# Kernel optimization log

Hardware: AMD Instinct MI355X
Metric: run time of the kernel (lower is better)

Reference implementation:

```python
import jax, jax.numpy as jnp
import numpy as np

B = 4096      # sessions
L = 32        # tokens per session (constant so sum(seq_len) == T)
T = B * L     # total tokens
H = 128       # hidden_size
HI = 8 * H    # input embedding dim (hidden_size * 8)


def setup_inputs() -> dict:
    key = jax.random.key(0)
    ks = jax.random.split(key, 8)
    s = lambda k, shape: jax.random.normal(k, shape, dtype=jnp.float32) * 0.02
    return {
        "inter_item_emb": s(ks[0], (T, HI)),
        "intra_item_emb": s(ks[1], (T, HI)),
        "seq_len": jnp.full((B,), L, dtype=jnp.int32),
        "Wf1_w": s(ks[2], (H, HI)), "Wf1_b": jnp.zeros((H,), jnp.float32),
        "Wf2_w": s(ks[3], (H, HI)), "Wf2_b": jnp.zeros((H,), jnp.float32),
        "W1_w": s(ks[4], (H, H)),   "W1_b": jnp.zeros((H,), jnp.float32),
        "W2_w": s(ks[5], (H, H)),   "W2_b": jnp.zeros((H,), jnp.float32),
        "q_w": s(ks[6], (1, H)),    "q_b": jnp.zeros((1,), jnp.float32),
        "W3_w": s(ks[7], (H, 2 * H)), "W3_b": jnp.zeros((H,), jnp.float32),
    }


def reference(inter_item_emb, intra_item_emb, seq_len,
              Wf1_w, Wf1_b, Wf2_w, Wf2_b,
              W1_w, W1_b, W2_w, W2_b,
              q_w, q_b, W3_w, W3_b):
    lin = lambda x, w, b: x @ w.T + b  # torch nn.Linear convention

    # item fusing: gated combination of the two projected embeddings
    f1 = lin(inter_item_emb, Wf1_w, Wf1_b)          # [T, H]
    f2 = lin(intra_item_emb, Wf2_w, Wf2_b)          # [T, H]
    gate = jax.nn.sigmoid(f1 + f2)
    h = f1 * gate + f2 * (1.0 - gate)               # [T, H]

    Ttok = h.shape[0]
    nseg = seq_len.shape[0]
    ends = jnp.cumsum(seq_len)                      # [B] exclusive ends
    # segment id of each token (sessions are contiguous row blocks)
    seg = jnp.searchsorted(ends, jnp.arange(Ttok), side="right")  # [T]
    last_idx = ends - 1                             # [B] last token of each session
    v_n = h[last_idx]                               # [B, H]

    # attention: alpha = q(sigmoid(W1(v_n_repeat) + W2(h)))
    w1v = lin(v_n, W1_w, W1_b)                      # [B, H], gather instead of repeat
    alpha = lin(jax.nn.sigmoid(w1v[seg] + lin(h, W2_w, W2_b)), q_w, q_b)  # [T, 1]

    # attention-weighted segment sum pooling
    s_g = jax.ops.segment_sum(alpha * h, seg, num_segments=nseg)  # [B, H]

    h_s = lin(jnp.concatenate([v_n, s_g], axis=1), W3_w, W3_b)    # [B, H]
    return h_s
```

## Files before the change

kernel.cpp:

```cpp
#include <hip/hip_runtime.h>
#include <hip/hip_bf16.h>

#define THREADS 512
#define HP 136

typedef float f32x4 __attribute__((ext_vector_type(4)));
typedef short s16x8 __attribute__((ext_vector_type(8)));

static __device__ __forceinline__ short f2b(float x) {
    return __builtin_bit_cast(short, __float2bfloat16(x));
}
static __device__ __forceinline__ float b2f(short u) {
    unsigned int v = ((unsigned int)(unsigned short)u) << 16;
    return __builtin_bit_cast(float, v);
}
static __device__ __forceinline__ void split8(const f32x4 a, const f32x4 b, s16x8& hi, s16x8& lo) {
    #pragma unroll
    for (int j = 0; j < 4; ++j) {
        short h0 = f2b(a[j]); hi[j]   = h0; lo[j]   = f2b(a[j] - b2f(h0));
        short h1 = f2b(b[j]); hi[j+4] = h1; lo[j+4] = f2b(b[j] - b2f(h1));
    }
}
static __device__ __forceinline__ s16x8 cvt8(const f32x4 a, const f32x4 b) {
    s16x8 r;
    r[0]=f2b(a[0]); r[1]=f2b(a[1]); r[2]=f2b(a[2]); r[3]=f2b(a[3]);
    r[4]=f2b(b[0]); r[5]=f2b(b[1]); r[6]=f2b(b[2]); r[7]=f2b(b[3]);
    return r;
}
static __device__ __forceinline__ float sigm(float x) { return 1.0f / (1.0f + __expf(-x)); }

#define MFMA16(A,B,C) __builtin_amdgcn_mfma_f32_16x16x32_bf16((A),(B),(C),0,0,0)

#define RAWBAR() do {                                               \
    asm volatile("s_waitcnt lgkmcnt(0)" ::: "memory");              \
    __builtin_amdgcn_s_barrier();                                   \
    asm volatile("" ::: "memory"); } while (0)

__global__ __launch_bounds__(256) void itemfusing_prep(
    const float* __restrict__ Wf1, const float* __restrict__ Wf2,
    const float* __restrict__ W2, short* __restrict__ wsp)
{
    const int t = blockIdx.x * 256 + threadIdx.x;
    if (t < 32768) {
        const int s  = t & 7;
        const int n  = (t >> 3) & 127;
        const int kc = (t >> 10) & 15;
        const int fz = (t >> 14) & 1;
        const int k  = kc * 64 + (s >> 2) * 32 + (s & 3) * 8;
        const float* src = (fz ? Wf2 : Wf1) + (size_t)n * 1024 + k;
        const int sp = s ^ (n & 7);
        *(s16x8*)(wsp + (size_t)(fz * 16 + kc) * 8192 + n * 64 + sp * 8)
            = cvt8(*(const f32x4*)src, *(const f32x4*)(src + 4));
    } else if (t < 32768 + 2048) {
        const int i = (t - 32768) * 8;
        const float* src = W2 + i;
        *(s16x8*)(wsp + 262144 + i) = cvt8(*(const f32x4*)src, *(const f32x4*)(src + 4));
    }
}

__global__ __launch_bounds__(THREADS, 2) void itemfusing_main(
    const float* __restrict__ inter, const float* __restrict__ intra,
    const float* __restrict__ bf1, const float* __restrict__ bf2,
    const float* __restrict__ W1,  const float* __restrict__ b1,
    const float* __restrict__ b2,
    const float* __restrict__ qw,  const float* __restrict__ qb,
    const float* __restrict__ W3,  const float* __restrict__ b3,
    const short* __restrict__ gimg, const short* __restrict__ w2b,
    float* __restrict__ out)
{
    __shared__ union {
        short wbuf[2][2][128][64];
        struct {
            short hbuf[4][32][HP];
            float vn [8][128];
            float w1v[8][128];
            float sgl[8][128];
        } t;
    } u;

    const int tid = threadIdx.x;
    const int w   = tid >> 6;
    const int l   = tid & 63;
    const int l15 = l & 15;
    const int kg  = l >> 4;
    const int sess = blockIdx.x * 8 + w;
    const int row0 = sess * 32;
    const int m7  = l15 & 7;
    const int s0p = (kg ^ m7) * 8;
    const int s1p = ((4 + kg) ^ m7) * 8;

    const float* A1 = inter + (size_t)(row0 + l15) * 1024 + kg * 8;
    const float* A2 = intra + (size_t)(row0 + l15) * 1024 + kg * 8;
    short* wb = &u.wbuf[0][0][0][0];

    f32x4 acc1[2][8], acc2[2][8];
    #pragma unroll
    for (int mt = 0; mt < 2; ++mt)
        #pragma unroll
        for (int nt = 0; nt < 8; ++nt) {
            acc1[mt][nt] = f32x4{0.f,0.f,0.f,0.f};
            acc2[mt][nt] = f32x4{0.f,0.f,0.f,0.f};
        }

    s16x8 wr0, wr1, wr2, wr3;
#define WLOADR(KC) do {                                                         \
    const short* p0_ = gimg + (size_t)(KC) * 8192 + tid * 8;                    \
    const short* p1_ = gimg + (size_t)(16 + (KC)) * 8192 + tid * 8;             \
    wr0 = *(const s16x8*)p0_;          wr1 = *(const s16x8*)(p0_ + 4096);       \
    wr2 = *(const s16x8*)p1_;          wr3 = *(const s16x8*)(p1_ + 4096); } while (0)
#define WSTORE(BUF) do {                                                        \
    short* d_ = wb + (BUF) * 16384 + tid * 8;                                   \
    *(s16x8*)d_ = wr0;           *(s16x8*)(d_ + 4096) = wr1;                    \
    *(s16x8*)(d_ + 8192) = wr2;  *(s16x8*)(d_ + 12288) = wr3; } while (0)

    f32x4 AE0, AE1, AE2, AE3, AE4, AE5, AE6, AE7;
    f32x4 AO0, AO1, AO2, AO3, AO4, AO5, AO6, AO7;
#define ALOAD(S, AP, KC) do {                                                   \
    const float* p_ = (AP) + (KC) * 64;                                         \
    S##0 = *(const f32x4*)p_;        S##1 = *(const f32x4*)(p_ + 4);            \
    S##2 = *(const f32x4*)(p_ + 32); S##3 = *(const f32x4*)(p_ + 36);           \
    const float* q_ = p_ + (size_t)16 * 1024;                                   \
    S##4 = *(const f32x4*)q_;        S##5 = *(const f32x4*)(q_ + 4);            \
    S##6 = *(const f32x4*)(q_ + 32); S##7 = *(const f32x4*)(q_ + 36); } while (0)

#define KSTEP(PB, ACC, AH0, AH1, AL0, AL1, SP) do {                             \
    _Pragma("unroll")                                                           \
    for (int nt_ = 0; nt_ < 8; ++nt_) {                                         \
        s16x8 bh_ = *(const s16x8*)((PB) + nt_ * 1024 + (SP));                  \
        ACC[0][nt_] = MFMA16(AH0, bh_, ACC[0][nt_]);                            \
        ACC[1][nt_] = MFMA16(AH1, bh_, ACC[1][nt_]);                            \
        ACC[0][nt_] = MFMA16(AL0, bh_, ACC[0][nt_]);                            \
        ACC[1][nt_] = MFMA16(AL1, bh_, ACC[1][nt_]);                            \
    } } while (0)

#define COMPUTE(BUF, FZ, ACC, S) do {                                           \
    const short* pb_ = wb + (BUF) * 16384 + (FZ) * 8192 + l15 * 64;             \
    s16x8 ah0, al0, ah1, al1;                                                   \
    split8(S##0, S##1, ah0, al0);                                               \
    split8(S##4, S##5, ah1, al1);                                               \
    KSTEP(pb_, ACC, ah0, ah1, al0, al1, s0p);                                   \
    split8(S##2, S##3, ah0, al0);                                               \
    split8(S##6, S##7, ah1, al1);                                               \
    KSTEP(pb_, ACC, ah0, ah1, al0, al1, s1p);                                   \
    } while (0)

    WLOADR(0); WSTORE(0);
    WLOADR(1);
    ALOAD(AE, A1, 0);
    ALOAD(AO, A2, 0);
    RAWBAR();

    #pragma unroll 1
    for (int kc = 0; kc < 16; ++kc) {
        const bool more = (kc < 15);
        if (more) WSTORE((kc + 1) & 1);
        if (kc < 14) WLOADR(kc + 2);
        COMPUTE(kc & 1, 0, acc1, AE);
        if (more) ALOAD(AE, A1, kc + 1);
        COMPUTE(kc & 1, 1, acc2, AO);
        if (more) ALOAD(AO, A2, kc + 1);
        RAWBAR();
    }
#undef WLOADR
#undef WSTORE
#undef ALOAD
#undef KSTEP
#undef COMPUTE

    #pragma unroll
    for (int nt = 0; nt < 8; ++nt) {
        const int n = nt * 16 + l15;
        const float bb1 = bf1[n], bb2 = bf2[n];
        #pragma unroll
        for (int mt = 0; mt < 2; ++mt)
            #pragma unroll
            for (int rj = 0; rj < 4; ++rj) {
                float x1 = acc1[mt][nt][rj] + bb1;
                float x2 = acc2[mt][nt][rj] + bb2;
                float g  = sigm(x1 + x2);
                acc1[mt][nt][rj] = x2 + g * (x1 - x2);
            }
    }

    if (kg == 3) {
        #pragma unroll
        for (int nt = 0; nt < 8; ++nt) u.t.vn[w][nt * 16 + l15] = acc1[1][nt][3];
    }
    asm volatile("s_waitcnt lgkmcnt(0)" ::: "memory");

    {
        const int n0 = l, n1 = l + 64;
        const float* w1r0 = W1 + (size_t)n0 * 128;
        const float* w1r1 = W1 + (size_t)n1 * 128;
        float s0 = 0.f, s1 = 0.f;
        #pragma unroll
        for (int kk = 0; kk < 128; kk += 4) {
            f32x4 vv = *(const f32x4*)&u.t.vn[w][kk];
            f32x4 u0 = *(const f32x4*)(w1r0 + kk);
            f32x4 u1 = *(const f32x4*)(w1r1 + kk);
            #pragma unroll
            for (int j = 0; j < 4; ++j) { s0 += u0[j] * vv[j]; s1 += u1[j] * vv[j]; }
        }
        u.t.w1v[w][n0] = s0 + b1[n0];
        u.t.w1v[w][n1] = s1 + b1[n1];
    }
    asm volatile("s_waitcnt lgkmcnt(0)" ::: "memory");

    auto tail = [&](int wj) {
        short (*hb)[HP] = u.t.hbuf[wj];
        #pragma unroll
        for (int nt = 0; nt < 8; ++nt)
            #pragma unroll
            for (int mt = 0; mt < 2; ++mt)
                #pragma unroll
                for (int rj = 0; rj < 4; ++rj)
                    hb[16 * mt + kg * 4 + rj][nt * 16 + l15] = f2b(acc1[mt][nt][rj]);
        asm volatile("s_waitcnt lgkmcnt(0)" ::: "memory");

        f32x4 accw[2][8];
        #pragma unroll
        for (int mt = 0; mt < 2; ++mt)
            #pragma unroll
            for (int nt = 0; nt < 8; ++nt) accw[mt][nt] = f32x4{0.f,0.f,0.f,0.f};
        #pragma unroll
        for (int ks = 0; ks < 4; ++ks) {
            const int kl = ks * 32 + kg * 8;
            s16x8 ah0 = *(const s16x8*)&hb[l15][kl];
            s16x8 ah1 = *(const s16x8*)&hb[16 + l15][kl];
            #pragma unroll
            for (int nt = 0; nt < 8; ++nt) {
                s16x8 bw = *(const s16x8*)&w2b[(size_t)(nt * 16 + l15) * 128 + kl];
                accw[0][nt] = MFMA16(ah0, bw, accw[0][nt]);
                accw[1][nt] = MFMA16(ah1, bw, accw[1][nt]);
            }
        }

        float part[2][4];
        #pragma unroll
        for (int mt = 0; mt < 2; ++mt)
            #pragma unroll
            for (int rj = 0; rj < 4; ++rj) part[mt][rj] = 0.f;
        #pragma unroll
        for (int nt = 0; nt < 8; ++nt) {
            const int n = nt * 16 + l15;
            const float qn = qw[n], wv_ = u.t.w1v[w][n], bb = b2[n];
            #pragma unroll
            for (int mt = 0; mt < 2; ++mt)
                #pragma unroll
                for (int rj = 0; rj < 4; ++rj)
                    part[mt][rj] += qn * sigm(wv_ + accw[mt][nt][rj] + bb);
        }
        const float qbias = qb[0];
        #pragma unroll
        for (int mt = 0; mt < 2; ++mt)
            #pragma unroll
            for (int rj = 0; rj < 4; ++rj) {
                float v = part[mt][rj];
                v += __shfl_xor(v, 1); v += __shfl_xor(v, 2);
                v += __shfl_xor(v, 4); v += __shfl_xor(v, 8);
                part[mt][rj] = v + qbias;
            }

        #pragma unroll
        for (int nt = 0; nt < 8; ++nt) {
            float s = 0.f;
            #pragma unroll
            for (int mt = 0; mt < 2; ++mt)
                #pragma unroll
                for (int rj = 0; rj < 4; ++rj)
                    s += part[mt][rj] * acc1[mt][nt][rj];
            s += __shfl_xor(s, 16);
            s += __shfl_xor(s, 32);
            if (l < 16) u.t.sgl[w][nt * 16 + l15] = s;
        }
        asm volatile("s_waitcnt lgkmcnt(0)" ::: "memory");

        const int n0 = l, n1 = l + 64;
        const float* w3r0 = W3 + (size_t)n0 * 256;
        const float* w3r1 = W3 + (size_t)n1 * 256;
        float h0 = b3[n0], h1 = b3[n1];
        #pragma unroll
        for (int kk = 0; kk < 128; kk += 4) {
            f32x4 vv = *(const f32x4*)&u.t.vn[w][kk];
            f32x4 ss = *(const f32x4*)&u.t.sgl[w][kk];
            f32x4 a0 = *(const f32x4*)(w3r0 + kk);
            f32x4 a1 = *(const f32x4*)(w3r1 + kk);
            f32x4 c0 = *(const f32x4*)(w3r0 + 128 + kk);
            f32x4 c1 = *(const f32x4*)(w3r1 + 128 + kk);
            #pragma unroll
            for (int j = 0; j < 4; ++j) {
                h0 += a0[j] * vv[j] + c0[j] * ss[j];
                h1 += a1[j] * vv[j] + c1[j] * ss[j];
            }
        }
        out[(size_t)sess * 128 + n0] = h0;
        out[(size_t)sess * 128 + n1] = h1;
    };

    if (w < 4) tail(w);
    __syncthreads();
    if (w >= 4) tail(w - 4);
}

__global__ __launch_bounds__(128) void itemfusing_naive(
    const float* __restrict__ inter, const float* __restrict__ intra,
    const float* __restrict__ Wf1, const float* __restrict__ bf1,
    const float* __restrict__ Wf2, const float* __restrict__ bf2,
    const float* __restrict__ W1,  const float* __restrict__ b1,
    const float* __restrict__ W2,  const float* __restrict__ b2,
    const float* __restrict__ qw,  const float* __restrict__ qb,
    const float* __restrict__ W3,  const float* __restrict__ b3,
    float* __restrict__ out)
{
    __shared__ float h[32][128];
    __shared__ float vn[128], w1v[128], al[32], sg[128], red[128];
    const int n = threadIdx.x; const int sess = blockIdx.x;
    for (int t0 = 0; t0 < 32; ++t0) {
        const float* e1 = inter + (size_t)(sess * 32 + t0) * 1024;
        const float* e2 = intra + (size_t)(sess * 32 + t0) * 1024;
        const float* r1 = Wf1 + (size_t)n * 1024;
        const float* r2 = Wf2 + (size_t)n * 1024;
        float s1 = bf1[n], s2 = bf2[n];
        for (int k = 0; k < 1024; ++k) { s1 += e1[k] * r1[k]; s2 += e2[k] * r2[k]; }
        float g = sigm(s1 + s2);
        h[t0][n] = s2 + g * (s1 - s2);
    }
    __syncthreads();
    vn[n] = h[31][n];
    __syncthreads();
    { float a = b1[n]; const float* w1r = W1 + (size_t)n * 128;
      for (int k = 0; k < 128; ++k) a += w1r[k] * vn[k];
      w1v[n] = a; }
    __syncthreads();
    for (int t0 = 0; t0 < 32; ++t0) {
        float x = b2[n]; const float* w2r = W2 + (size_t)n * 128;
        for (int k = 0; k < 128; ++k) x += w2r[k] * h[t0][k];
        red[n] = qw[n] * sigm(w1v[n] + x); __syncthreads();
        for (int s_ = 64; s_ > 0; s_ >>= 1) { if (n < s_) red[n] += red[n + s_]; __syncthreads(); }
        if (n == 0) al[t0] = red[0] + qb[0];
        __syncthreads();
    }
    { float s = 0.f; for (int t0 = 0; t0 < 32; ++t0) s += al[t0] * h[t0][n];
      sg[n] = s; }
    __syncthreads();
    { float o = b3[n]; const float* w3r = W3 + (size_t)n * 256;
      for (int k = 0; k < 128; ++k) o += w3r[k] * vn[k] + w3r[128 + k] * sg[k];
      out[(size_t)sess * 128 + n] = o; }
}

extern "C" void kernel_launch(void* const* d_in, const int* in_sizes, int n_in,
                              void* d_out, int out_size, void* d_ws, size_t ws_size,
                              hipStream_t stream) {
    (void)n_in; (void)out_size;
    const float* inter = (const float*)d_in[0];
    const float* intra = (const float*)d_in[1];
    const float* Wf1   = (const float*)d_in[3];
    const float* bf1   = (const float*)d_in[4];
    const float* Wf2   = (const float*)d_in[5];
    const float* bf2   = (const float*)d_in[6];
    const float* W1    = (const float*)d_in[7];
    const float* b1    = (const float*)d_in[8];
    const float* W2    = (const float*)d_in[9];
    const float* b2    = (const float*)d_in[10];
    const float* qw    = (const float*)d_in[11];
    const float* qb    = (const float*)d_in[12];
    const float* W3    = (const float*)d_in[13];
    const float* b3    = (const float*)d_in[14];
    float* out = (float*)d_out;

    const int nsess = in_sizes[2];
    const size_t WS_NEED = (size_t)(262144 + 16384) * sizeof(short);

    if (d_ws != nullptr && ws_size >= WS_NEED) {
        short* wsp = (short*)d_ws;
        itemfusing_prep<<<136, 256, 0, stream>>>(Wf1, Wf2, W2, wsp);
        itemfusing_main<<<nsess / 8, THREADS, 0, stream>>>(
            inter, intra, bf1, bf2, W1, b1, b2, qw, qb, W3, b3,
            wsp, wsp + 262144, out);
    } else {
        itemfusing_naive<<<nsess, 128, 0, stream>>>(
            inter, intra, Wf1, bf1, Wf2, bf2, W1, b1, W2, b2, qw, qb, W3, b3, out);
    }
}
```

Baseline: 324.4 us.

## Halve block to four sessions per block and split weight staging into halves

Each block now has 256 threads and handles four sessions instead of eight, so there are twice as many blocks. Because fewer threads share the load, the per-k-chunk weight staging into LDS is split into two halves (A and B) that are loaded and stored at different points inside the compute loop. Both activation loads are moved to after the second compute. This aims to improve occupancy and spread the weight-staging latency, but each weight tile is now reused by half as many sessions, which doubles the global and LDS weight traffic per token.

```diff
diff --git a/kernel.cpp b/kernel.cpp
--- a/kernel.cpp
+++ b/kernel.cpp
@@ -1,7 +1,7 @@
 #include <hip/hip_runtime.h>
 #include <hip/hip_bf16.h>
 
-#define THREADS 512
+#define THREADS 256
 #define HP 136
 
 typedef float f32x4 __attribute__((ext_vector_type(4)));
@@ -71,10 +71,10 @@
     __shared__ union {
         short wbuf[2][2][128][64];
         struct {
-            short hbuf[4][32][HP];
-            float vn [8][128];
-            float w1v[8][128];
-            float sgl[8][128];
+            short hbuf[2][32][HP];
+            float vn [4][128];
+            float w1v[4][128];
+            float sgl[4][128];
         } t;
     } u;
 
@@ -83,7 +83,7 @@
     const int l   = tid & 63;
     const int l15 = l & 15;
     const int kg  = l >> 4;
-    const int sess = blockIdx.x * 8 + w;
+    const int sess = blockIdx.x * 4 + w;
     const int row0 = sess * 32;
     const int m7  = l15 & 7;
     const int s0p = (kg ^ m7) * 8;
@@ -102,16 +102,24 @@
             acc2[mt][nt] = f32x4{0.f,0.f,0.f,0.f};
         }
 
-    s16x8 wr0, wr1, wr2, wr3;
-#define WLOADR(KC) do {                                                         \
-    const short* p0_ = gimg + (size_t)(KC) * 8192 + tid * 8;                    \
-    const short* p1_ = gimg + (size_t)(16 + (KC)) * 8192 + tid * 8;             \
-    wr0 = *(const s16x8*)p0_;          wr1 = *(const s16x8*)(p0_ + 4096);       \
-    wr2 = *(const s16x8*)p1_;          wr3 = *(const s16x8*)(p1_ + 4096); } while (0)
-#define WSTORE(BUF) do {                                                        \
+    s16x8 wa0, wa1, wa2, wa3;
+    s16x8 wb0, wb1, wb2, wb3;
+#define WL_A(KC) do {                                                           \
+    const short* p_ = gimg + (size_t)(KC) * 8192 + tid * 8;                     \
+    wa0 = *(const s16x8*)p_;          wa1 = *(const s16x8*)(p_ + 2048);         \
+    wa2 = *(const s16x8*)(p_ + 4096); wa3 = *(const s16x8*)(p_ + 6144); } while (0)
+#define WL_B(KC) do {                                                           \
+    const short* p_ = gimg + (size_t)(16 + (KC)) * 8192 + tid * 8;              \
+    wb0 = *(const s16x8*)p_;          wb1 = *(const s16x8*)(p_ + 2048);         \
+    wb2 = *(const s16x8*)(p_ + 4096); wb3 = *(const s16x8*)(p_ + 6144); } while (0)
+#define WS_A(BUF) do {                                                          \
     short* d_ = wb + (BUF) * 16384 + tid * 8;                                   \
-    *(s16x8*)d_ = wr0;           *(s16x8*)(d_ + 4096) = wr1;                    \
-    *(s16x8*)(d_ + 8192) = wr2;  *(s16x8*)(d_ + 12288) = wr3; } while (0)
+    *(s16x8*)d_ = wa0;           *(s16x8*)(d_ + 2048) = wa1;                    \
+    *(s16x8*)(d_ + 4096) = wa2;  *(s16x8*)(d_ + 6144) = wa3; } while (0)
+#define WS_B(BUF) do {                                                          \
+    short* d_ = wb + (BUF) * 16384 + 8192 + tid * 8;                            \
+    *(s16x8*)d_ = wb0;           *(s16x8*)(d_ + 2048) = wb1;                    \
+    *(s16x8*)(d_ + 4096) = wb2;  *(s16x8*)(d_ + 6144) = wb3; } while (0)
 
     f32x4 AE0, AE1, AE2, AE3, AE4, AE5, AE6, AE7;
     f32x4 AO0, AO1, AO2, AO3, AO4, AO5, AO6, AO7;
@@ -144,8 +152,9 @@
     KSTEP(pb_, ACC, ah0, ah1, al0, al1, s1p);                                   \
     } while (0)
 
-    WLOADR(0); WSTORE(0);
-    WLOADR(1);
+    WL_A(0); WS_A(0);
+    WL_B(0); WS_B(0);
+    WL_A(1);
     ALOAD(AE, A1, 0);
     ALOAD(AO, A2, 0);
     RAWBAR();
@@ -153,16 +162,19 @@
     #pragma unroll 1
     for (int kc = 0; kc < 16; ++kc) {
         const bool more = (kc < 15);
-        if (more) WSTORE((kc + 1) & 1);
-        if (kc < 14) WLOADR(kc + 2);
+        if (more) WS_A((kc + 1) & 1);
+        if (more) WL_B(kc + 1);
         COMPUTE(kc & 1, 0, acc1, AE);
-        if (more) ALOAD(AE, A1, kc + 1);
+        if (more) WS_B((kc + 1) & 1);
+        if (kc < 14) WL_A(kc + 2);
         COMPUTE(kc & 1, 1, acc2, AO);
-        if (more) ALOAD(AO, A2, kc + 1);
+        if (more) { ALOAD(AE, A1, kc + 1); ALOAD(AO, A2, kc + 1); }
         RAWBAR();
     }
-#undef WLOADR
-#undef WSTORE
+#undef WL_A
+#undef WL_B
+#undef WS_A
+#undef WS_B
 #undef ALOAD
 #undef KSTEP
 #undef COMPUTE
@@ -297,9 +309,9 @@
         out[(size_t)sess * 128 + n1] = h1;
     };
 
-    if (w < 4) tail(w);
-    __syncthreads();
-    if (w >= 4) tail(w - 4);
+    if (w < 2) tail(w);
+    __syncthreads();
+    if (w >= 2) tail(w - 2);
 }
 
 __global__ __launch_bounds__(128) void itemfusing_naive(
@@ -374,7 +386,7 @@
     if (d_ws != nullptr && ws_size >= WS_NEED) {
         short* wsp = (short*)d_ws;
         itemfusing_prep<<<136, 256, 0, stream>>>(Wf1, Wf2, W2, wsp);
-        itemfusing_main<<<nsess / 8, THREADS, 0, stream>>>(
+        itemfusing_main<<<nsess / 4, THREADS, 0, stream>>>(
             inter, intra, bf1, bf2, W1, b1, b2, qw, qb, W3, b3,
             wsp, wsp + 262144, out);
     } else {
```

Measured after the change: 425.8 us. +31.3%, slower.
